# Performance work log

Hardware: AMD Instinct MI355X
Metric: run time of the kernel (lower is better)

## Reference

```python
import jax, jax.numpy as jnp
import numpy as np

VOCAB = 128

def setup_inputs() -> dict:
    key = jax.random.key(0)
    k1, k2, k3, k4 = jax.random.split(key, 4)
    B, S, H = 64, 512, 1024
    x = jax.random.randint(k1, (B, S), 0, VOCAB, dtype=jnp.int32)
    h = jnp.zeros((B, H), dtype=jnp.float32)
    # Xavier-normal-ish scaled params
    W_xh = jax.random.normal(k2, (VOCAB, H), dtype=jnp.float32) * (2.0 / (VOCAB + H)) ** 0.5
    W_hh = jax.random.normal(k3, (H, H), dtype=jnp.float32) * (1.0 / H) ** 0.5
    b_h = jnp.zeros((H,), dtype=jnp.float32)
    W_out = jax.random.normal(k4, (H, VOCAB), dtype=jnp.float32) * (1.0 / H) ** 0.5
    b_out = jnp.zeros((VOCAB,), dtype=jnp.float32)
    return {"x": x, "h": h, "W_xh": W_xh, "W_hh": W_hh, "b_h": b_h,
            "W_out": W_out, "b_out": b_out}

def reference(x, h, W_xh, W_hh, b_h, W_out, b_out):
    """x: (B,S) int32, h: (B,H). Returns (logits (B,S,V), h_final (B,H)).
    one_hot(x) @ W_xh == embedding gather W_xh[x] (same math, no dense one-hot).
    Dropout is identity (eval mode). Sequential tanh recurrence via lax.scan."""
    x_emb = W_xh[x]                      # (B, S, H) gather == one-hot matmul
    x_emb_t = jnp.swapaxes(x_emb, 0, 1)  # (S, B, H) scan over time

    def step(h, xe):
        h_new = jnp.tanh(xe + h @ W_hh + b_h)
        return h_new, h_new

    h_final, hidden = jax.lax.scan(step, h, x_emb_t)  # hidden: (S, B, H)
    hidden = jnp.swapaxes(hidden, 0, 1)               # (B, S, H)
    logits = hidden @ W_out + b_out                   # (B, S, V)
    return logits, h_final
```

## Files before the change

### kernel.cpp

```cpp
#include <hip/hip_runtime.h>
#include <hip/hip_bf16.h>
#include <stdint.h>


#define Bz 64
#define Sz 512
#define Hz 1024
#define Vz 128
#define NWG 64
#define COLS 32
#define WGT 512

typedef __attribute__((ext_vector_type(8)))  short short8;
typedef __attribute__((ext_vector_type(16))) float f32x16;
typedef __attribute__((ext_vector_type(4)))  unsigned u32x4;
typedef __attribute__((ext_vector_type(2)))  unsigned u32x2;

__device__ unsigned g_epoch;

__device__ __align__(16) unsigned g_hx[3][2][64][64][8];
__device__ __align__(16) unsigned short g_hidden[(size_t)Sz*2*64*64*8];
__device__ __align__(16) unsigned short g_wout[64*4*64*8];

__device__ __forceinline__ unsigned short f2bf(float f) {
  union { float f; unsigned u; } v; v.f = f;
  unsigned r = v.u + 0x7FFFu + ((v.u >> 16) & 1u);
  return (unsigned short)(r >> 16);
}

__device__ __forceinline__ float fast_tanh(float x) {
  float cx = fminf(9.0f, fmaxf(-9.0f, x));
  float e  = __builtin_amdgcn_exp2f(cx * 2.88539008178f);
  return (e - 1.0f) * __builtin_amdgcn_rcpf(e + 1.0f);
}

__device__ __forceinline__ void load16_seq(const unsigned* p0, u32x4 t[16]) {
  const unsigned* p1 = p0 + 1024;
  const unsigned* p2 = p0 + 2048;
  const unsigned* p3 = p0 + 3072;
  asm volatile(
    "global_load_dwordx4 %0,  %16, off sc1\n\t"
    "global_load_dwordx4 %1,  %16, off offset:16 sc1\n\t"
    "global_load_dwordx4 %2,  %16, off offset:2048 sc1\n\t"
    "global_load_dwordx4 %3,  %16, off offset:2064 sc1\n\t"
    "global_load_dwordx4 %4,  %17, off sc1\n\t"
    "global_load_dwordx4 %5,  %17, off offset:16 sc1\n\t"
    "global_load_dwordx4 %6,  %17, off offset:2048 sc1\n\t"
    "global_load_dwordx4 %7,  %17, off offset:2064 sc1\n\t"
    "global_load_dwordx4 %8,  %18, off sc1\n\t"
    "global_load_dwordx4 %9,  %18, off offset:16 sc1\n\t"
    "global_load_dwordx4 %10, %18, off offset:2048 sc1\n\t"
    "global_load_dwordx4 %11, %18, off offset:2064 sc1\n\t"
    "global_load_dwordx4 %12, %19, off sc1\n\t"
    "global_load_dwordx4 %13, %19, off offset:16 sc1\n\t"
    "global_load_dwordx4 %14, %19, off offset:2048 sc1\n\t"
    "global_load_dwordx4 %15, %19, off offset:2064 sc1\n\t"
    "s_waitcnt vmcnt(0)"
    : "=&v"(t[0]), "=&v"(t[1]), "=&v"(t[2]),  "=&v"(t[3]),
      "=&v"(t[4]), "=&v"(t[5]), "=&v"(t[6]),  "=&v"(t[7]),
      "=&v"(t[8]), "=&v"(t[9]), "=&v"(t[10]), "=&v"(t[11]),
      "=&v"(t[12]),"=&v"(t[13]),"=&v"(t[14]), "=&v"(t[15])
    : "v"(p0), "v"(p1), "v"(p2), "v"(p3)
    : "memory");
}

__device__ __forceinline__ void store8_sc1(unsigned* p, u32x2 v) {
  asm volatile("global_store_dwordx2 %0, %1, off sc1" :: "v"(p), "v"(v) : "memory");
}

__global__ void pack_wout(const float* __restrict__ W_out) {
  if (blockIdx.x == 0 && threadIdx.x == 0) g_epoch = g_epoch + 1u;
  int gid = blockIdx.x * blockDim.x + threadIdx.x;
  int lane = gid & 63;
  int nt   = (gid >> 6) & 3;
  int kb   = gid >> 8;
  int n = nt * 32 + (lane & 31);
  int k0 = kb * 16 + (lane >> 5) * 8;
  unsigned short t[8];
#pragma unroll
  for (int j = 0; j < 8; ++j)
    t[j] = f2bf(W_out[(size_t)(k0 + j) * Vz + n]);
  uint4 w;
  w.x = (unsigned)t[0] | ((unsigned)t[1] << 16);
  w.y = (unsigned)t[2] | ((unsigned)t[3] << 16);
  w.z = (unsigned)t[4] | ((unsigned)t[5] << 16);
  w.w = (unsigned)t[6] | ((unsigned)t[7] << 16);
  *(uint4*)&g_wout[(size_t)gid * 8] = w;
}

__global__ __launch_bounds__(WGT) void rnn_persistent(
    const int* __restrict__ x, const float* __restrict__ h0,
    const float* __restrict__ W_xh, const float* __restrict__ W_hh,
    const float* __restrict__ b_h, float* __restrict__ out)
{
  __shared__ unsigned short ldsW[64 * 64 * 8];
  __shared__ float red[8 * 1024];

  const int g    = blockIdx.x;
  const int bh   = g >> 5;
  const int cg   = g & 31;
  const int n0g  = cg * COLS;
  const int tid  = threadIdx.x;
  const int lane = tid & 63;
  const int ki   = tid >> 6;
  const int bn   = lane & 31;
  const unsigned epb = g_epoch << 10;

  for (int idx = tid; idx < 64 * 64; idx += WGT) {
    int kb = idx >> 6, L = idx & 63;
    int n = L & 31, kq = L >> 5;
    unsigned short t[8];
#pragma unroll
    for (int j = 0; j < 8; ++j)
      t[j] = f2bf(W_hh[(size_t)(kb * 16 + kq * 8 + j) * Hz + n0g + n]);
    uint4 w;
    w.x = (unsigned)t[0] | ((unsigned)t[1] << 16);
    w.y = (unsigned)t[2] | ((unsigned)t[3] << 16);
    w.z = (unsigned)t[4] | ((unsigned)t[5] << 16);
    w.w = (unsigned)t[6] | ((unsigned)t[7] << 16);
    *(uint4*)&ldsW[(size_t)idx * 8] = w;
  }

  {
    int u  = g * 512 + tid;
    int w  = u & 3;
    int L  = (u >> 2) & 63;
    int kb = (u >> 8) & 63;
    int fb = (u >> 14) & 1;
    int m  = fb * 32 + (L & 31);
    int k  = kb * 16 + (L >> 5) * 8 + w * 2;
    const float* src = &h0[(size_t)m * Hz + k];
    u32x2 v;
    v.x = (unsigned)f2bf(src[0]) | ((unsigned)f2bf(src[1]) << 16);
    v.y = epb + 1u;
    store8_sc1(&g_hx[0][fb][kb][L][2 * w], v);
  }
  __syncthreads();

  const int er   = tid & 31;
  const int em   = bh * 32 + er;
  const int c0   = (tid >> 5) * 2;
  const int kcol = n0g + c0;
  const int kb_g = kcol >> 4;
  const int kq2  = (kcol >> 3) & 1;
  const int lslot = kq2 * 32 + er;
  const int wq   = (c0 >> 1) & 3;
  unsigned* exw0 = &g_hx[0][bh][kb_g][lslot][2 * wq];
  const size_t hidOff =
      ((((size_t)bh * 64) + kb_g) * 64 + lslot) * 8 + (kcol & 7);
  const float bias0 = b_h[kcol], bias1 = b_h[kcol + 1];

  int tok_n = x[em * Sz];
  float2 xv_n = *(const float2*)&W_xh[(size_t)tok_n * Hz + kcol];

  int rp = 0;
  for (int s = 0; s < Sz; ++s) {
    const int wp = (rp == 2) ? 0 : rp + 1;
    const unsigned tgt = epb + (unsigned)(s + 1);

    u32x4 t[16];
    {
      const unsigned* hp = &g_hx[rp][bh][ki * 8][lane][0];
      const int bound = (s == 0) ? 65536 : 8192;
      for (int it = 0; it < bound; ++it) {
        load16_seq(hp, t);
        unsigned bad = (t[0].y ^ tgt) | (t[0].w ^ tgt);
#pragma unroll
        for (int i = 1; i < 16; ++i)
          bad |= (t[i].y ^ tgt) | (t[i].w ^ tgt);
        if (__all(bad == 0u)) break;
        __builtin_amdgcn_s_sleep(1);
      }
      asm volatile("" ::: "memory");
    }

    f32x16 acc0 = {}, acc1 = {};
#pragma unroll
    for (int p = 0; p < 8; p += 2) {
      u32x4 fa, fb2;
      fa.x  = t[2 * p].x;     fa.y  = t[2 * p].z;
      fa.z  = t[2 * p + 1].x; fa.w  = t[2 * p + 1].z;
      fb2.x = t[2 * p + 2].x; fb2.y = t[2 * p + 2].z;
      fb2.z = t[2 * p + 3].x; fb2.w = t[2 * p + 3].z;
      const int kbp = ki * 8 + p;
      short8 ba = *(const short8*)&ldsW[(size_t)(kbp * 64 + lane) * 8];
      short8 bb = *(const short8*)&ldsW[(size_t)((kbp + 1) * 64 + lane) * 8];
      acc0 = __builtin_amdgcn_mfma_f32_32x32x16_bf16(*(short8*)&fa, ba,
                                                     acc0, 0, 0, 0);
      acc1 = __builtin_amdgcn_mfma_f32_32x32x16_bf16(*(short8*)&fb2, bb,
                                                     acc1, 0, 0, 0);
    }

    float2 xv = xv_n;
    if (s + 1 < Sz) {
      int t2 = x[em * Sz + s + 1];
      xv_n = *(const float2*)&W_xh[(size_t)t2 * Hz + kcol];
    }

    __syncthreads();
    {
#pragma unroll
      for (int r = 0; r < 16; ++r) {
        int m = 4 * (lane >> 5) + (r & 3) + 8 * (r >> 2);
        red[ki * 1024 + m * 32 + (bn ^ m)] = acc0[r] + acc1[r];
      }
    }
    __syncthreads();

    float z0, z1;
    {
      const int o0 = er * 32 + (c0 ^ er);
      const int o1 = er * 32 + ((c0 + 1) ^ er);
      z0 = ((red[o0] + red[1024 + o0]) + (red[2048 + o0] + red[3072 + o0])) +
           ((red[4096 + o0] + red[5120 + o0]) + (red[6144 + o0] + red[7168 + o0]));
      z1 = ((red[o1] + red[1024 + o1]) + (red[2048 + o1] + red[3072 + o1])) +
           ((red[4096 + o1] + red[5120 + o1]) + (red[6144 + o1] + red[7168 + o1]));
    }
    z0 = fast_tanh(z0 + xv.x + bias0);
    z1 = fast_tanh(z1 + xv.y + bias1);

    unsigned w2 = (unsigned)f2bf(z0) | ((unsigned)f2bf(z1) << 16);

    u32x2 v; v.x = w2; v.y = epb + (unsigned)(s + 2);
    store8_sc1(exw0 + (size_t)wp * 65536, v);

    *(unsigned*)&g_hidden[(size_t)s * 65536 + hidOff] = w2;
    if (s == Sz - 1) {
      float* hf = out + (size_t)Bz * Sz * Vz + (size_t)em * Hz + kcol;
      hf[0] = z0; hf[1] = z1;
    }
    rp = wp;
  }
}

__global__ __launch_bounds__(256) void logits_gemm(
    const float* __restrict__ b_out, float* __restrict__ out)
{
  const int tid = threadIdx.x, lane = tid & 63, nt = tid >> 6;
  const int s = blockIdx.x >> 1, mi = blockIdx.x & 1;
  const unsigned short* ab = &g_hidden[((size_t)s * 8192 + (size_t)mi * 4096) * 8];

  f32x16 acc = {};
#pragma unroll 8
  for (int kb = 0; kb < 64; ++kb) {
    short8 a = *(const short8*)&ab[(size_t)(kb * 64 + lane) * 8];
    short8 b = *(const short8*)&g_wout[(size_t)((kb * 4 + nt) * 64 + lane) * 8];
    acc = __builtin_amdgcn_mfma_f32_32x32x16_bf16(a, b, acc, 0, 0, 0);
  }
  const int col = nt * 32 + (lane & 31);
  const float bo = b_out[col];
  const int rbase = 4 * (lane >> 5);
#pragma unroll
  for (int r = 0; r < 16; ++r) {
    int m = rbase + (r & 3) + 8 * (r >> 2);
    int em = mi * 32 + m;
    out[((size_t)em * Sz + s) * Vz + col] = acc[r] + bo;
  }
}

extern "C" void kernel_launch(void* const* d_in, const int* in_sizes, int n_in,
                              void* d_out, int out_size, void* d_ws, size_t ws_size,
                              hipStream_t stream) {
  const int*   x     = (const int*)d_in[0];
  const float* h0    = (const float*)d_in[1];
  const float* W_xh  = (const float*)d_in[2];
  const float* W_hh  = (const float*)d_in[3];
  const float* b_h   = (const float*)d_in[4];
  const float* W_out = (const float*)d_in[5];
  const float* b_out = (const float*)d_in[6];
  float* out = (float*)d_out;

  pack_wout<<<64, 256, 0, stream>>>(W_out);
  rnn_persistent<<<NWG, WGT, 0, stream>>>(x, h0, W_xh, W_hh, b_h, out);
  logits_gemm<<<Sz * 2, 256, 0, stream>>>(b_out, out);
}
```

Measured before the change: 1.980 ms.

## Add per-wave progress flags to gate polling before loading tagged hidden state

Each wave publishes a per-step progress flag in workspace memory after writing its slice of the hidden state. Consumers now spin on 32 small flag words before issuing the full tagged 16-vector load, instead of repeatedly reloading the whole tile and checking tags. The per-step __syncthreads calls become raw s_barrier with sched_barrier fences and an explicit lgkmcnt wait, which removes extra implicit waits. This adds a memset, an extra atomic store per wave per step and a second polling phase. The flag store is relaxed and has no ordering against the data store, so the tag check is kept as a fallback.

```diff
diff --git a/kernel.cpp b/kernel.cpp
--- a/kernel.cpp
+++ b/kernel.cpp
@@ -91,7 +91,8 @@
 __global__ __launch_bounds__(WGT) void rnn_persistent(
     const int* __restrict__ x, const float* __restrict__ h0,
     const float* __restrict__ W_xh, const float* __restrict__ W_hh,
-    const float* __restrict__ b_h, float* __restrict__ out)
+    const float* __restrict__ b_h, float* __restrict__ out,
+    unsigned* __restrict__ flags)
 {
   __shared__ unsigned short ldsW[64 * 64 * 8];
   __shared__ float red[8 * 1024];
@@ -136,6 +137,9 @@
     store8_sc1(&g_hx[0][fb][kb][L][2 * w], v);
   }
   __syncthreads();
+  if (lane == 0)
+    __hip_atomic_store(&flags[(g * 8 + ki) * 4], 1u, __ATOMIC_RELAXED,
+                       __HIP_MEMORY_SCOPE_AGENT);
 
   const int er   = tid & 31;
   const int em   = bh * 32 + er;
@@ -150,19 +154,34 @@
       ((((size_t)bh * 64) + kb_g) * 64 + lslot) * 8 + (kcol & 7);
   const float bias0 = b_h[kcol], bias1 = b_h[kcol + 1];
 
+  const int pflag =
+      ((bh * 32 + ki * 4 + (lane >> 3)) * 8 + (lane & 7)) * 4;
+
   int tok_n = x[em * Sz];
   float2 xv_n = *(const float2*)&W_xh[(size_t)tok_n * Hz + kcol];
 
   int rp = 0;
   for (int s = 0; s < Sz; ++s) {
     const int wp = (rp == 2) ? 0 : rp + 1;
-    const unsigned tgt = epb + (unsigned)(s + 1);
+    const unsigned ftgt = (unsigned)(s + 1);
+    const unsigned tgt  = epb + (unsigned)(s + 1);
+
+    {
+      const int bound = (s == 0) ? 131072 : 32768;
+      for (int it = 0; it < bound; ++it) {
+        unsigned v = 0xFFFFFFFFu;
+        if (lane < 32)
+          v = __hip_atomic_load(&flags[pflag], __ATOMIC_RELAXED,
+                                __HIP_MEMORY_SCOPE_AGENT);
+        if (__all(v >= ftgt)) break;
+      }
+      asm volatile("" ::: "memory");
+    }
 
     u32x4 t[16];
     {
       const unsigned* hp = &g_hx[rp][bh][ki * 8][lane][0];
-      const int bound = (s == 0) ? 65536 : 8192;
-      for (int it = 0; it < bound; ++it) {
+      for (int rt = 0; rt < 8192; ++rt) {
         load16_seq(hp, t);
         unsigned bad = (t[0].y ^ tgt) | (t[0].w ^ tgt);
 #pragma unroll
@@ -197,7 +216,10 @@
       xv_n = *(const float2*)&W_xh[(size_t)t2 * Hz + kcol];
     }
 
-    __syncthreads();
+    __builtin_amdgcn_sched_barrier(0);
+    __builtin_amdgcn_s_barrier();
+    __builtin_amdgcn_sched_barrier(0);
+
     {
 #pragma unroll
       for (int r = 0; r < 16; ++r) {
@@ -205,7 +227,10 @@
         red[ki * 1024 + m * 32 + (bn ^ m)] = acc0[r] + acc1[r];
       }
     }
-    __syncthreads();
+    asm volatile("s_waitcnt lgkmcnt(0)" ::: "memory");
+    __builtin_amdgcn_sched_barrier(0);
+    __builtin_amdgcn_s_barrier();
+    __builtin_amdgcn_sched_barrier(0);
 
     float z0, z1;
     {
@@ -223,6 +248,9 @@
 
     u32x2 v; v.x = w2; v.y = epb + (unsigned)(s + 2);
     store8_sc1(exw0 + (size_t)wp * 65536, v);
+    if (lane == 0)
+      __hip_atomic_store(&flags[(g * 8 + ki) * 4], (unsigned)(s + 2),
+                         __ATOMIC_RELAXED, __HIP_MEMORY_SCOPE_AGENT);
 
     *(unsigned*)&g_hidden[(size_t)s * 65536 + hidOff] = w2;
     if (s == Sz - 1) {
@@ -270,7 +298,9 @@
   const float* b_out = (const float*)d_in[6];
   float* out = (float*)d_out;
 
+  (void)hipMemsetAsync(d_ws, 0, 8192, stream);
   pack_wout<<<64, 256, 0, stream>>>(W_out);
-  rnn_persistent<<<NWG, WGT, 0, stream>>>(x, h0, W_xh, W_hh, b_h, out);
+  rnn_persistent<<<NWG, WGT, 0, stream>>>(x, h0, W_xh, W_hh, b_h, out,
+                                          (unsigned*)d_ws);
   logits_gemm<<<Sz * 2, 256, 0, stream>>>(b_out, out);
 }
```

New measurement: 2.160 ms. +9.1%, slower.
